# Kernel tuning notes

Measured on AMD Instinct MI355X. Metric: run time of the kernel, lower is better.

Reference implementation:

```python
import jax, jax.numpy as jnp
import numpy as np

NHEAD = 8
LN_EPS = 1e-5   # torch nn.LayerNorm default
ATT_EPS = 1e-6  # LinearAttention eps


def layernorm(x, g, b):
    mu = jnp.mean(x, axis=-1, keepdims=True)
    var = jnp.mean((x - mu) ** 2, axis=-1, keepdims=True)
    return (x - mu) / jnp.sqrt(var + LN_EPS) * g + b


def setup_inputs() -> dict:
    key = jax.random.key(0)
    ks = jax.random.split(key, 9)
    B, C, H, W = 8, 256, 64, 64
    d = C
    w = lambda k, shp: (jax.random.normal(k, shp, dtype=jnp.float32) * 0.02)
    return {
        "x": jax.random.normal(ks[0], (B, C, H, W), dtype=jnp.float32),
        "source": jax.random.normal(ks[1], (B, C, H, W), dtype=jnp.float32),
        # weights stored [in, out] (already transposed vs torch's [out, in])
        "Wq": w(ks[2], (d, d)),
        "Wk": w(ks[3], (d, d)),
        "Wv": w(ks[4], (d, d)),
        "Wm": w(ks[5], (d, d)),
        "W1": w(ks[6], (2 * d, 2 * d)),
        "W2": w(ks[7], (2 * d, d)),
        "g1": jnp.ones((d,), jnp.float32),
        "b1": jnp.zeros((d,), jnp.float32),
        "g2": jnp.ones((d,), jnp.float32),
        "b2": jnp.zeros((d,), jnp.float32),
    }


def reference(x, source, Wq, Wk, Wv, Wm, W1, W2, g1, b1, g2, b2):
    B, C, H, W = x.shape
    L = H * W
    dim = C // NHEAD
    xs = x.reshape(B, C, L).transpose(0, 2, 1)        # [B, L, C]
    ss = source.reshape(B, C, L).transpose(0, 2, 1)   # [B, L, C]

    q = (xs @ Wq).reshape(B, L, NHEAD, dim)
    k = (ss @ Wk).reshape(B, L, NHEAD, dim)
    v = (ss @ Wv).reshape(B, L, NHEAD, dim)

    # linear attention with elu+1 feature map
    Q = jax.nn.elu(q) + 1.0
    K = jax.nn.elu(k) + 1.0
    vals = v / L
    KV = jnp.einsum('nshd,nshv->nhdv', K, vals)                    # [B, h, d, d]
    Z = 1.0 / (jnp.einsum('nlhd,nhd->nlh', Q, K.sum(axis=1)) + ATT_EPS)
    msg = jnp.einsum('nlhd,nhdv,nlh->nlhv', Q, KV, Z) * L          # [B, L, h, d]

    msg = msg.reshape(B, L, C) @ Wm
    msg = layernorm(msg, g1, b1)
    msg = jax.nn.relu(jnp.concatenate([xs, msg], axis=-1) @ W1) @ W2
    msg = layernorm(msg, g2, b2)

    out = xs + msg
    return out.transpose(0, 2, 1).reshape(B, C, H, W)
```

## Files before the change

### kernel.cpp

```cpp
#include <hip/hip_runtime.h>

typedef unsigned short u16;
typedef __bf16 bf16x8 __attribute__((ext_vector_type(8)));
typedef float f32x4 __attribute__((ext_vector_type(4)));

__device__ __forceinline__ u16 f2bf(float f) {
  unsigned int u = __float_as_uint(f);
  u += 0x7fffu + ((u >> 16) & 1u);
  return (u16)(u >> 16);
}
__device__ __forceinline__ float bf2f(u16 v) {
  return __uint_as_float(((unsigned)v) << 16);
}

#define GLDS16(gp, lp)                                                   \
  __builtin_amdgcn_global_load_lds(                                      \
      (const __attribute__((address_space(1))) unsigned int*)(gp),       \
      (__attribute__((address_space(3))) unsigned int*)(lp), 16, 0, 0)

#define OFF_WQ     0u
#define OFF_WK     131072u
#define OFF_WV     262144u
#define OFF_WM     393216u
#define OFF_W1     524288u
#define OFF_W2     1048576u
#define OFF_CAT    1310720u
#define OFF_SSB    34865152u
#define OFF_KVPROJ 68419584u
#define OFF_KV     152305664u
#define OFF_KS     152567808u
#define OFF_KVP    152576000u
#define OFF_KSP    154673152u

__global__ __launch_bounds__(256) void transpose_in_kernel(
    const float* __restrict__ x, const float* __restrict__ srcp,
    u16* __restrict__ cat, u16* __restrict__ ssb) {
  __shared__ float s[32][33];
  int z = blockIdx.z;
  const float* src = z < 8 ? x : srcp;
  u16* dst = z < 8 ? cat : ssb;
  int dstride = z < 8 ? 512 : 256;
  int b = z & 7;
  int lt = blockIdx.x * 32, ct = blockIdx.y * 32;
  int tx = threadIdx.x & 31, ty = threadIdx.x >> 5;
#pragma unroll
  for (int i = 0; i < 4; ++i)
    s[ty + i * 8][tx] = src[((size_t)b * 256 + ct + ty + i * 8) * 4096 + lt + tx];
  __syncthreads();
#pragma unroll
  for (int i = 0; i < 4; ++i)
    dst[((size_t)b * 4096 + lt + ty + i * 8) * dstride + ct + tx] = f2bf(s[tx][ty + i * 8]);
}

__global__ __launch_bounds__(256) void wprep_all_kernel(
    const float* __restrict__ Wq, const float* __restrict__ Wk,
    const float* __restrict__ Wv, const float* __restrict__ Wm,
    const float* __restrict__ W1, const float* __restrict__ W2,
    u16* __restrict__ dq, u16* __restrict__ dk, u16* __restrict__ dv,
    u16* __restrict__ dm, u16* __restrict__ d1, u16* __restrict__ d2) {
  __shared__ float s[32][33];
  int bid = blockIdx.x;
  const float* src; u16* dst; int Kd, Nd, t;
  if (bid < 64)       { src = Wq; dst = dq; Kd = 256; Nd = 256; t = bid; }
  else if (bid < 128) { src = Wk; dst = dk; Kd = 256; Nd = 256; t = bid - 64; }
  else if (bid < 192) { src = Wv; dst = dv; Kd = 256; Nd = 256; t = bid - 128; }
  else if (bid < 256) { src = Wm; dst = dm; Kd = 256; Nd = 256; t = bid - 192; }
  else if (bid < 512) { src = W1; dst = d1; Kd = 512; Nd = 512; t = bid - 256; }
  else                { src = W2; dst = d2; Kd = 512; Nd = 256; t = bid - 512; }
  int ntn = Nd >> 5;
  int kt = (t / ntn) * 32, nt = (t % ntn) * 32;
  int tx = threadIdx.x & 31, ty = threadIdx.x >> 5;
#pragma unroll
  for (int i = 0; i < 4; ++i)
    s[ty + i * 8][tx] = src[(size_t)(kt + ty + i * 8) * Nd + nt + tx];
  __syncthreads();
#pragma unroll
  for (int i = 0; i < 4; ++i)
    dst[(size_t)(nt + ty + i * 8) * Kd + kt + tx] = f2bf(s[tx][ty + i * 8]);
}

template <int EPI>
__global__ __launch_bounds__(512) void gemm256_kernel(
    const u16* __restrict__ A, int lda, const u16* __restrict__ Wt, int K,
    u16* __restrict__ outp, int ldo) {
  __shared__ alignas(16) u16 sA[128 * 64];
  __shared__ alignas(16) u16 sB[256 * 64];
  const int t = threadIdx.x;
  int bid = blockIdx.x;
  int xcd = bid & 7, i0 = bid >> 3;
  const int m0 = (xcd * 32 + (i0 >> 1)) * 128;
  const int n0 = (i0 & 1) * 256;
  const int w = t >> 6, lane = t & 63;
  const int wm = (w >> 2) * 64, wn = (w & 3) * 64;
  const int lr = lane & 15, lk = lane >> 4;
  f32x4 acc[4][4] = {};
  const int nkt = K >> 6;
  for (int kt = 0; kt < nkt; ++kt) {
    __syncthreads();
#pragma unroll
    for (int i = 0; i < 2; ++i) {
      int id = t + i * 512, row = id >> 3, ch = (id & 7) << 3;
      GLDS16(A + (size_t)(m0 + row) * lda + kt * 64 + ch, sA + id * 8);
    }
#pragma unroll
    for (int i = 0; i < 4; ++i) {
      int id = t + i * 512, row = id >> 3, ch = (id & 7) << 3;
      GLDS16(Wt + (size_t)(n0 + row) * K + kt * 64 + ch, sB + id * 8);
    }
    __syncthreads();
    bf16x8 af[4][2], bfr[4][2];
#pragma unroll
    for (int f = 0; f < 4; ++f) {
#pragma unroll
      for (int ks = 0; ks < 2; ++ks) {
        af[f][ks] = *reinterpret_cast<const bf16x8*>(
            &sA[(wm + f * 16 + lr) * 64 + ks * 32 + lk * 8]);
        bfr[f][ks] = *reinterpret_cast<const bf16x8*>(
            &sB[(wn + f * 16 + lr) * 64 + ks * 32 + lk * 8]);
      }
    }
#pragma unroll
    for (int ks = 0; ks < 2; ++ks)
#pragma unroll
      for (int fm = 0; fm < 4; ++fm)
#pragma unroll
        for (int fn = 0; fn < 4; ++fn)
          acc[fm][fn] = __builtin_amdgcn_mfma_f32_16x16x32_bf16(
              af[fm][ks], bfr[fn][ks], acc[fm][fn], 0, 0, 0);
  }
  const int r0 = (lane >> 4) * 4, c0 = lane & 15;
#pragma unroll
  for (int fm = 0; fm < 4; ++fm) {
#pragma unroll
    for (int fn = 0; fn < 4; ++fn) {
      int gr = m0 + wm + fm * 16 + r0;
      int gc = n0 + wn + fn * 16 + c0;
#pragma unroll
      for (int r = 0; r < 4; ++r) {
        float v = acc[fm][fn][r];
        if (EPI == 3) v = v > 0.f ? v : 0.f;
        if (EPI == 4) v = (gc < 256) ? (v > 0.f ? v + 1.f : __expf(v)) : v * (1.f / 4096.f);
        outp[(size_t)(gr + r) * ldo + gc] = f2bf(v);
      }
    }
  }
}

__global__ __launch_bounds__(256) void kv_partial_kernel(
    const u16* __restrict__ KVproj, float* __restrict__ KVp,
    float* __restrict__ KSp) {
  __shared__ alignas(16) float sK[64][32];
  __shared__ alignas(16) float sV[64][32];
  const int bh = blockIdx.x, sl = blockIdx.y;
  const int b = bh >> 3, h = bh & 7;
  const int t = threadIdx.x;
  const int lrow = t >> 2, lcol = (t & 3) * 8;
  const int d = t >> 3, vg = (t & 7) * 4;
  float a0 = 0, a1 = 0, a2 = 0, a3 = 0, ks = 0;
  for (int lt = 0; lt < 512; lt += 64) {
    __syncthreads();
    size_t roff = ((size_t)b * 4096 + sl * 512 + lt + lrow) * 512 + h * 32 + lcol;
    uint4 kq = *reinterpret_cast<const uint4*>(KVproj + roff);
    uint4 vq = *reinterpret_cast<const uint4*>(KVproj + roff + 256);
    float* dk = &sK[lrow][lcol];
    float* dv = &sV[lrow][lcol];
#pragma unroll
    for (int j = 0; j < 4; ++j) {
      unsigned uk = ((const unsigned*)&kq)[j];
      unsigned uv = ((const unsigned*)&vq)[j];
      dk[2 * j] = __uint_as_float(uk << 16);
      dk[2 * j + 1] = __uint_as_float(uk & 0xffff0000u);
      dv[2 * j] = __uint_as_float(uv << 16);
      dv[2 * j + 1] = __uint_as_float(uv & 0xffff0000u);
    }
    __syncthreads();
#pragma unroll 8
    for (int i = 0; i < 64; ++i) {
      float kd = sK[i][d];
      a0 += kd * sV[i][vg + 0];
      a1 += kd * sV[i][vg + 1];
      a2 += kd * sV[i][vg + 2];
      a3 += kd * sV[i][vg + 3];
      ks += kd;
    }
  }
  float* o = KVp + (size_t)sl * 65536 + bh * 1024 + d * 32 + vg;
  o[0] = a0; o[1] = a1; o[2] = a2; o[3] = a3;
  if ((t & 7) == 0) KSp[(size_t)sl * 2048 + bh * 32 + d] = ks;
}

__global__ __launch_bounds__(256) void kv_reduce_kernel(
    const float* __restrict__ KVp, const float* __restrict__ KSp,
    float* __restrict__ KV, float* __restrict__ Ksum) {
  int gid = blockIdx.x * 256 + threadIdx.x;
  if (gid < 65536) {
    float s = 0;
#pragma unroll
    for (int i = 0; i < 8; ++i) s += KVp[(size_t)i * 65536 + gid];
    KV[gid] = s;
  } else if (gid - 65536 < 2048) {
    int j = gid - 65536;
    float s = 0;
#pragma unroll
    for (int i = 0; i < 8; ++i) s += KSp[(size_t)i * 2048 + j];
    Ksum[j] = s;
  }
}

__global__ __launch_bounds__(256) void wcomb_kernel(
    const float* __restrict__ KVb, const u16* __restrict__ wmt,
    u16* __restrict__ wc) {
  const int bid = blockIdx.x;
  const int b = bid >> 8, n = bid & 255;
  const int k = threadIdx.x, h = k >> 5, d = k & 31;
  const float* kv = KVb + ((size_t)b * 8 + h) * 1024 + d * 32;
  const u16* wm = wmt + (size_t)n * 256 + h * 32;
  float s = 0.f;
#pragma unroll
  for (int v = 0; v < 32; ++v) s += kv[v] * bf2f(wm[v]);
  wc[((size_t)b * 256 + n) * 256 + k] = f2bf(s);
}

__global__ __launch_bounds__(256) void qmsg_kernel(
    const u16* __restrict__ cat, const u16* __restrict__ WqT,
    const float* __restrict__ KSb, const u16* __restrict__ wc,
    const float* __restrict__ g1, const float* __restrict__ b1,
    u16* __restrict__ catout) {
  __shared__ alignas(16) char smem[57344];
  u16* sA = (u16*)smem;
  u16* sB = (u16*)(smem + 8192);
  u16* Qlds = (u16*)smem;
  float* scr = (float*)(smem + 33280);
  u16* sWc = (u16*)(smem + 40960);
  u16* T = (u16*)smem;
  const int t = threadIdx.x;
  const int m0 = blockIdx.x * 64;
  const int b = m0 >> 12;
  const int w = t >> 6, lane = t & 63;
  const int lr = lane & 15, lk = lane >> 4;
  const int wn = w * 64;
  f32x4 acc[4][4] = {};
  float ksv[4];
#pragma unroll
  for (int fn = 0; fn < 4; ++fn) ksv[fn] = KSb[b * 256 + wn + fn * 16 + lr];
  for (int kt = 0; kt < 4; ++kt) {
    __syncthreads();
#pragma unroll
    for (int i = 0; i < 2; ++i) {
      int id = t + i * 256, row = id >> 3, ch = (id & 7) * 8;
      GLDS16(cat + (size_t)(m0 + row) * 512 + kt * 64 + ch, sA + id * 8);
    }
#pragma unroll
    for (int i = 0; i < 8; ++i) {
      int id = t + i * 256, row = id >> 3, ch = (id & 7) * 8;
      GLDS16(WqT + (size_t)row * 256 + kt * 64 + ch, sB + id * 8);
    }
    __syncthreads();
    bf16x8 af[4][2], bfr[4][2];
#pragma unroll
    for (int f = 0; f < 4; ++f)
#pragma unroll
      for (int ks = 0; ks < 2; ++ks) {
        af[f][ks] = *(const bf16x8*)&sA[(f * 16 + lr) * 64 + ks * 32 + lk * 8];
        bfr[f][ks] = *(const bf16x8*)&sB[(wn + f * 16 + lr) * 64 + ks * 32 + lk * 8];
      }
#pragma unroll
    for (int ks = 0; ks < 2; ++ks)
#pragma unroll
      for (int fm = 0; fm < 4; ++fm)
#pragma unroll
        for (int fn = 0; fn < 4; ++fn)
          acc[fm][fn] = __builtin_amdgcn_mfma_f32_16x16x32_bf16(
              af[fm][ks], bfr[fn][ks], acc[fm][fn], 0, 0, 0);
  }
#pragma unroll
  for (int fm = 0; fm < 4; ++fm)
#pragma unroll
    for (int r = 0; r < 4; ++r) {
      float q[4];
#pragma unroll
      for (int fn = 0; fn < 4; ++fn) {
        float v = acc[fm][fn][r];
        q[fn] = v > 0.f ? v + 1.f : __expf(v);
      }
      float zd0 = q[0] * ksv[0] + q[1] * ksv[1];
      float zd1 = q[2] * ksv[2] + q[3] * ksv[3];
#pragma unroll
      for (int off = 1; off < 16; off <<= 1) {
        zd0 += __shfl_xor(zd0, off);
        zd1 += __shfl_xor(zd1, off);
      }
      float z0 = 4096.f / (zd0 + 1e-6f);
      float z1 = 4096.f / (zd1 + 1e-6f);
      acc[fm][0][r] = q[0] * z0; acc[fm][1][r] = q[1] * z0;
      acc[fm][2][r] = q[2] * z1; acc[fm][3][r] = q[3] * z1;
    }
  __syncthreads();
#pragma unroll
  for (int fm = 0; fm < 4; ++fm)
#pragma unroll
    for (int fn = 0; fn < 4; ++fn)
#pragma unroll
      for (int r = 0; r < 4; ++r)
        Qlds[(fm * 16 + lk * 4 + r) * 260 + wn + fn * 16 + lr] = f2bf(acc[fm][fn][r]);
  f32x4 acc2[4][4] = {};
  const u16* Bw = wc + (size_t)b * 65536;
  for (int kc = 0; kc < 8; ++kc) {
    __syncthreads();
#pragma unroll
    for (int i = 0; i < 4; ++i) {
      int id = t + i * 256, row = id >> 2, ch = (id & 3) * 8;
      GLDS16(Bw + (size_t)row * 256 + kc * 32 + (ch ^ ((row & 3) << 3)), sWc + id * 8);
    }
    __syncthreads();
    bf16x8 a2[4], b2f[4];
#pragma unroll
    for (int f = 0; f < 4; ++f)
      a2[f] = *(const bf16x8*)&Qlds[(f * 16 + lr) * 260 + kc * 32 + lk * 8];
#pragma unroll
    for (int fn = 0; fn < 4; ++fn) {
      int br = wn + fn * 16 + lr;
      b2f[fn] = *(const bf16x8*)&sWc[br * 32 + ((lk * 8) ^ ((br & 3) << 3))];
    }
#pragma unroll
    for (int fm = 0; fm < 4; ++fm)
#pragma unroll
      for (int fn = 0; fn < 4; ++fn)
        acc2[fm][fn] = __builtin_amdgcn_mfma_f32_16x16x32_bf16(
            a2[fm], b2f[fn], acc2[fm][fn], 0, 0, 0);
  }
#pragma unroll
  for (int fm = 0; fm < 4; ++fm)
#pragma unroll
    for (int r = 0; r < 4; ++r) {
      float s = 0.f, sq = 0.f;
#pragma unroll
      for (int fn = 0; fn < 4; ++fn) {
        float a = acc2[fm][fn][r];
        s += a; sq += a * a;
      }
#pragma unroll
      for (int off = 1; off < 16; off <<= 1) {
        s += __shfl_xor(s, off);
        sq += __shfl_xor(sq, off);
      }
      if (lr == 0) {
        int row = fm * 16 + lk * 4 + r;
        scr[row * 8 + w * 2] = s;
        scr[row * 8 + w * 2 + 1] = sq;
      }
    }
  __syncthreads();
  float gvs[4], bvs[4];
#pragma unroll
  for (int fn = 0; fn < 4; ++fn) {
    gvs[fn] = g1[wn + fn * 16 + lr];
    bvs[fn] = b1[wn + fn * 16 + lr];
  }
#pragma unroll
  for (int fm = 0; fm < 4; ++fm)
#pragma unroll
    for (int r = 0; r < 4; ++r) {
      int row = fm * 16 + lk * 4 + r;
      float s = 0.f, sq = 0.f;
#pragma unroll
      for (int j = 0; j < 4; ++j) {
        s += scr[row * 8 + j * 2];
        sq += scr[row * 8 + j * 2 + 1];
      }
      float mu = s * (1.f / 256.f);
      float var = sq * (1.f / 256.f) - mu * mu;
      float rstd = rsqrtf(var + 1e-5f);
#pragma unroll
      for (int fn = 0; fn < 4; ++fn) {
        float y = (acc2[fm][fn][r] - mu) * rstd * gvs[fn] + bvs[fn];
        T[(fm * 16 + lk * 4 + r) * 260 + wn + fn * 16 + lr] = f2bf(y);
      }
    }
  __syncthreads();
#pragma unroll
  for (int i = 0; i < 8; ++i) {
    int idx = t + i * 256;
    int row = idx >> 5, c16 = idx & 31;
    uint4 val = *reinterpret_cast<const uint4*>(&T[row * 260 + c16 * 8]);
    *reinterpret_cast<uint4*>(catout + (size_t)(m0 + row) * 512 + 256 + c16 * 8) = val;
  }
}

__global__ __launch_bounds__(512) void mlp2_tail_kernel(
    const u16* __restrict__ hidden, const u16* __restrict__ W2T,
    const float* __restrict__ g2, const float* __restrict__ b2,
    const u16* __restrict__ catp, float* __restrict__ out) {
  __shared__ alignas(16) char smem[16384 + 32768 + 4096 + 2048];
  u16* sA = (u16*)smem;
  u16* sB = (u16*)(smem + 16384);
  float* scr = (float*)(smem + 49152);
  float* sG = (float*)(smem + 53248);
  float* T = (float*)smem;
  const int t = threadIdx.x;
  const int m0 = blockIdx.x * 128;
  const int b = m0 >> 12, l0 = m0 & 4095;
  if (t < 256) { sG[t] = g2[t]; sG[256 + t] = b2[t]; }
  const int w = t >> 6, lane = t & 63;
  const int wm = (w >> 2) * 64, wn = (w & 3) * 64;
  const int lr = lane & 15, lk = lane >> 4;
  f32x4 acc[4][4] = {};
  for (int kt = 0; kt < 8; ++kt) {
    __syncthreads();
#pragma unroll
    for (int i = 0; i < 2; ++i) {
      int id = t + i * 512, row = id >> 3, chn = (id & 7) << 3;
      GLDS16(hidden + (size_t)(m0 + row) * 512 + kt * 64 + chn, sA + id * 8);
    }
#pragma unroll
    for (int i = 0; i < 4; ++i) {
      int id = t + i * 512, row = id >> 3, chn = (id & 7) << 3;
      GLDS16(W2T + (size_t)row * 512 + kt * 64 + chn, sB + id * 8);
    }
    __syncthreads();
    bf16x8 af[4][2], bfr[4][2];
#pragma unroll
    for (int f = 0; f < 4; ++f) {
#pragma unroll
      for (int ks = 0; ks < 2; ++ks) {
        af[f][ks] = *reinterpret_cast<const bf16x8*>(
            &sA[(wm + f * 16 + lr) * 64 + ks * 32 + lk * 8]);
        bfr[f][ks] = *reinterpret_cast<const bf16x8*>(
            &sB[(wn + f * 16 + lr) * 64 + ks * 32 + lk * 8]);
      }
    }
#pragma unroll
    for (int ks = 0; ks < 2; ++ks)
#pragma unroll
      for (int fm = 0; fm < 4; ++fm)
#pragma unroll
        for (int fn = 0; fn < 4; ++fn)
          acc[fm][fn] = __builtin_amdgcn_mfma_f32_16x16x32_bf16(
              af[fm][ks], bfr[fn][ks], acc[fm][fn], 0, 0, 0);
  }
#pragma unroll
  for (int fm = 0; fm < 4; ++fm)
#pragma unroll
    for (int r = 0; r < 4; ++r) {
      float s = 0.f, sq = 0.f;
#pragma unroll
      for (int fn = 0; fn < 4; ++fn) {
        float a = acc[fm][fn][r];
        s += a; sq += a * a;
      }
#pragma unroll
      for (int off = 1; off < 16; off <<= 1) {
        s += __shfl_xor(s, off);
        sq += __shfl_xor(sq, off);
      }
      if (lr == 0) {
        int row = wm + fm * 16 + lk * 4 + r;
        scr[row * 8 + (w & 3) * 2] = s;
        scr[row * 8 + (w & 3) * 2 + 1] = sq;
      }
    }
  __syncthreads();
  float gvs[4], bvs[4];
#pragma unroll
  for (int fn = 0; fn < 4; ++fn) {
    gvs[fn] = sG[wn + fn * 16 + lr];
    bvs[fn] = sG[256 + wn + fn * 16 + lr];
  }
#pragma unroll
  for (int fm = 0; fm < 4; ++fm)
#pragma unroll
    for (int r = 0; r < 4; ++r) {
      int row = wm + fm * 16 + lk * 4 + r;
      float s = 0.f, sq = 0.f;
#pragma unroll
      for (int j = 0; j < 4; ++j) {
        s += scr[row * 8 + j * 2];
        sq += scr[row * 8 + j * 2 + 1];
      }
      float mu = s * (1.f / 256.f);
      float var = sq * (1.f / 256.f) - mu * mu;
      float rstd = rsqrtf(var + 1e-5f);
#pragma unroll
      for (int fn = 0; fn < 4; ++fn) {
        float xs = bf2f(catp[(size_t)(m0 + row) * 512 + wn + fn * 16 + lr]);
        acc[fm][fn][r] = (acc[fm][fn][r] - mu) * rstd * gvs[fn] + bvs[fn] + xs;
      }
    }
  __syncthreads();
  for (int cc = 0; cc < 4; ++cc) {
    if ((w & 3) == cc) {
#pragma unroll
      for (int fm = 0; fm < 4; ++fm)
#pragma unroll
        for (int fn = 0; fn < 4; ++fn)
#pragma unroll
          for (int r = 0; r < 4; ++r)
            T[(fn * 16 + lr) * 129 + wm + fm * 16 + lk * 4 + r] = acc[fm][fn][r];
    }
    __syncthreads();
#pragma unroll
    for (int i = 0; i < 4; ++i) {
      int idx = t + i * 512;
      int cT = idx >> 5, lq = (idx & 31) * 4;
      int cg = cc * 64 + cT;
      size_t o = ((size_t)b * 256 + cg) * 4096 + l0 + lq;
      float4 ov;
      ov.x = T[cT * 129 + lq];
      ov.y = T[cT * 129 + lq + 1];
      ov.z = T[cT * 129 + lq + 2];
      ov.w = T[cT * 129 + lq + 3];
      *reinterpret_cast<float4*>(out + o) = ov;
    }
    __syncthreads();
  }
}

extern "C" void kernel_launch(void* const* d_in, const int* in_sizes, int n_in,
                              void* d_out, int out_size, void* d_ws, size_t ws_size,
                              hipStream_t stream) {
  (void)in_sizes; (void)n_in; (void)out_size; (void)ws_size;
  const float* x = (const float*)d_in[0];
  const float* srcp = (const float*)d_in[1];
  const float* Wq = (const float*)d_in[2];
  const float* Wk = (const float*)d_in[3];
  const float* Wv = (const float*)d_in[4];
  const float* Wm = (const float*)d_in[5];
  const float* W1 = (const float*)d_in[6];
  const float* W2 = (const float*)d_in[7];
  const float* g1 = (const float*)d_in[8];
  const float* b1 = (const float*)d_in[9];
  const float* g2 = (const float*)d_in[10];
  const float* b2 = (const float*)d_in[11];
  float* out = (float*)d_out;
  char* ws = (char*)d_ws;

  u16* wqt = (u16*)(ws + OFF_WQ);
  u16* wkvt = (u16*)(ws + OFF_WK);
  u16* wkt = (u16*)(ws + OFF_WK);
  u16* wvt = (u16*)(ws + OFF_WV);
  u16* wmt = (u16*)(ws + OFF_WM);
  u16* w1t = (u16*)(ws + OFF_W1);
  u16* w2t = (u16*)(ws + OFF_W2);
  u16* cat = (u16*)(ws + OFF_CAT);
  u16* ssb = (u16*)(ws + OFF_SSB);
  u16* kvproj = (u16*)(ws + OFF_KVPROJ);
  float* KVb = (float*)(ws + OFF_KV);
  float* KSb = (float*)(ws + OFF_KS);
  float* KVp = (float*)(ws + OFF_KVP);
  float* KSp = (float*)(ws + OFF_KSP);
  u16* hidden = kvproj;
  u16* wcombT = (u16*)(ws + OFF_KVP);

  dim3 blk(256);
  wprep_all_kernel<<<dim3(640), blk, 0, stream>>>(Wq, Wk, Wv, Wm, W1, W2,
                                                  wqt, wkt, wvt, wmt, w1t, w2t);
  transpose_in_kernel<<<dim3(128, 8, 16), blk, 0, stream>>>(x, srcp, cat, ssb);
  gemm256_kernel<4><<<dim3(512), dim3(512), 0, stream>>>(ssb, 256, wkvt, 256, kvproj, 512);
  kv_partial_kernel<<<dim3(64, 8), blk, 0, stream>>>(kvproj, KVp, KSp);
  kv_reduce_kernel<<<dim3(264), blk, 0, stream>>>(KVp, KSp, KVb, KSb);
  wcomb_kernel<<<dim3(2048), blk, 0, stream>>>(KVb, wmt, wcombT);
  qmsg_kernel<<<dim3(512), blk, 0, stream>>>(cat, wqt, KSb, wcombT, g1, b1, cat);
  gemm256_kernel<3><<<dim3(512), dim3(512), 0, stream>>>(cat, 512, w1t, 512, hidden, 512);
  mlp2_tail_kernel<<<dim3(256), dim3(512), 0, stream>>>(hidden, w2t, g2, b2, cat, out);
}
```

Baseline: 161.1 us.

## Fuse KV reduce with Wm combine, widen qmsg tile, vectorize input transpose

The input transpose moves to 64x64 tiles with float4 loads and packed 16-byte bf16 stores. The KV partial reduction and the KV·Wm combine are merged into one kernel that keeps reduced KV in shared memory, which removes a launch and the global KV round trip. The qmsg kernel now processes 128 rows per block with 512 threads, stages Q through LDS in two halves, and writes LayerNorm output directly to global memory instead of through an LDS transpose. In exchange, the fused reduce runs on only 64 blocks, and the direct stores are narrower and less coalesced.

```diff
diff --git a/kernel.cpp b/kernel.cpp
--- a/kernel.cpp
+++ b/kernel.cpp
@@ -27,29 +27,48 @@
 #define OFF_CAT    1310720u
 #define OFF_SSB    34865152u
 #define OFF_KVPROJ 68419584u
-#define OFF_KV     152305664u
 #define OFF_KS     152567808u
 #define OFF_KVP    152576000u
 #define OFF_KSP    154673152u
+#define OFF_WC     154740736u
 
 __global__ __launch_bounds__(256) void transpose_in_kernel(
     const float* __restrict__ x, const float* __restrict__ srcp,
     u16* __restrict__ cat, u16* __restrict__ ssb) {
-  __shared__ float s[32][33];
-  int z = blockIdx.z;
+  __shared__ float s[64][65];
+  const int z = blockIdx.z;
   const float* src = z < 8 ? x : srcp;
   u16* dst = z < 8 ? cat : ssb;
-  int dstride = z < 8 ? 512 : 256;
-  int b = z & 7;
-  int lt = blockIdx.x * 32, ct = blockIdx.y * 32;
-  int tx = threadIdx.x & 31, ty = threadIdx.x >> 5;
-#pragma unroll
-  for (int i = 0; i < 4; ++i)
-    s[ty + i * 8][tx] = src[((size_t)b * 256 + ct + ty + i * 8) * 4096 + lt + tx];
+  const int dstride = z < 8 ? 512 : 256;
+  const int b = z & 7;
+  const int lt = blockIdx.x * 64, ct = blockIdx.y * 64;
+  const int t = threadIdx.x;
+  const int cl = t >> 2, loff = (t & 3) * 16;
+#pragma unroll
+  for (int j = 0; j < 4; ++j) {
+    float4 v = *reinterpret_cast<const float4*>(
+        src + ((size_t)b * 256 + ct + cl) * 4096 + lt + loff + j * 4);
+    s[cl][loff + j * 4 + 0] = v.x;
+    s[cl][loff + j * 4 + 1] = v.y;
+    s[cl][loff + j * 4 + 2] = v.z;
+    s[cl][loff + j * 4 + 3] = v.w;
+  }
   __syncthreads();
 #pragma unroll
-  for (int i = 0; i < 4; ++i)
-    dst[((size_t)b * 4096 + lt + ty + i * 8) * dstride + ct + tx] = f2bf(s[tx][ty + i * 8]);
+  for (int i = 0; i < 2; ++i) {
+    int id = t + i * 256;
+    int ll = id >> 3, cg = id & 7;
+    unsigned pk[4];
+#pragma unroll
+    for (int j = 0; j < 4; ++j) {
+      unsigned lo = f2bf(s[cg * 8 + j * 2][ll]);
+      unsigned hi = f2bf(s[cg * 8 + j * 2 + 1][ll]);
+      pk[j] = lo | (hi << 16);
+    }
+    uint4 val = {pk[0], pk[1], pk[2], pk[3]};
+    *reinterpret_cast<uint4*>(
+        dst + ((size_t)b * 4096 + lt + ll) * dstride + ct + cg * 8) = val;
+  }
 }
 
 __global__ __launch_bounds__(256) void wprep_all_kernel(
@@ -189,56 +208,74 @@
   if ((t & 7) == 0) KSp[(size_t)sl * 2048 + bh * 32 + d] = ks;
 }
 
-__global__ __launch_bounds__(256) void kv_reduce_kernel(
+__global__ __launch_bounds__(256) void kvred_wcomb_kernel(
     const float* __restrict__ KVp, const float* __restrict__ KSp,
-    float* __restrict__ KV, float* __restrict__ Ksum) {
-  int gid = blockIdx.x * 256 + threadIdx.x;
-  if (gid < 65536) {
-    float s = 0;
-#pragma unroll
-    for (int i = 0; i < 8; ++i) s += KVp[(size_t)i * 65536 + gid];
-    KV[gid] = s;
-  } else if (gid - 65536 < 2048) {
-    int j = gid - 65536;
-    float s = 0;
-#pragma unroll
-    for (int i = 0; i < 8; ++i) s += KSp[(size_t)i * 2048 + j];
-    Ksum[j] = s;
-  }
-}
-
-__global__ __launch_bounds__(256) void wcomb_kernel(
-    const float* __restrict__ KVb, const u16* __restrict__ wmt,
-    u16* __restrict__ wc) {
-  const int bid = blockIdx.x;
-  const int b = bid >> 8, n = bid & 255;
-  const int k = threadIdx.x, h = k >> 5, d = k & 31;
-  const float* kv = KVb + ((size_t)b * 8 + h) * 1024 + d * 32;
-  const u16* wm = wmt + (size_t)n * 256 + h * 32;
-  float s = 0.f;
-#pragma unroll
-  for (int v = 0; v < 32; ++v) s += kv[v] * bf2f(wm[v]);
-  wc[((size_t)b * 256 + n) * 256 + k] = f2bf(s);
-}
-
-__global__ __launch_bounds__(256) void qmsg_kernel(
+    const u16* __restrict__ wmt, u16* __restrict__ wc,
+    float* __restrict__ Ksum) {
+  __shared__ float sKV[8 * 1032];
+  const int b = blockIdx.x >> 3, nc = blockIdx.x & 7;
+  const int t = threadIdx.x;
+#pragma unroll
+  for (int i = 0; i < 32; ++i) {
+    int idx = t + i * 256;
+    float s = 0.f;
+#pragma unroll
+    for (int sl = 0; sl < 8; ++sl) s += KVp[(size_t)sl * 65536 + b * 8192 + idx];
+    sKV[(idx >> 10) * 1032 + (idx & 1023)] = s;
+  }
+  if (nc == 0) {
+    float s = 0.f;
+#pragma unroll
+    for (int sl = 0; sl < 8; ++sl) s += KSp[(size_t)sl * 2048 + b * 256 + t];
+    Ksum[b * 256 + t] = s;
+  }
+  __syncthreads();
+  const int n = nc * 32 + (t >> 3), h = t & 7;
+  float wmv[32];
+  const u16* wmrow = wmt + (size_t)n * 256 + h * 32;
+#pragma unroll
+  for (int v = 0; v < 32; ++v) wmv[v] = bf2f(wmrow[v]);
+  unsigned pk[16];
+  const float* kvh = &sKV[h * 1032];
+#pragma unroll
+  for (int dp = 0; dp < 16; ++dp) {
+    unsigned lohi[2];
+#pragma unroll
+    for (int e = 0; e < 2; ++e) {
+      int d = dp * 2 + e;
+      const float* kv = kvh + d * 32;
+      float s = 0.f;
+#pragma unroll
+      for (int v = 0; v < 32; ++v) s += kv[v] * wmv[v];
+      lohi[e] = f2bf(s);
+    }
+    pk[dp] = lohi[0] | (lohi[1] << 16);
+  }
+  uint4* dst = (uint4*)(wc + ((size_t)b * 256 + n) * 256 + h * 32);
+#pragma unroll
+  for (int j = 0; j < 4; ++j) {
+    uint4 val = {pk[j * 4], pk[j * 4 + 1], pk[j * 4 + 2], pk[j * 4 + 3]};
+    dst[j] = val;
+  }
+}
+
+__global__ __launch_bounds__(512) void qmsg_kernel(
     const u16* __restrict__ cat, const u16* __restrict__ WqT,
     const float* __restrict__ KSb, const u16* __restrict__ wc,
     const float* __restrict__ g1, const float* __restrict__ b1,
     u16* __restrict__ catout) {
   __shared__ alignas(16) char smem[57344];
   u16* sA = (u16*)smem;
-  u16* sB = (u16*)(smem + 8192);
+  u16* sB = (u16*)(smem + 16384);
   u16* Qlds = (u16*)smem;
-  float* scr = (float*)(smem + 33280);
-  u16* sWc = (u16*)(smem + 40960);
-  u16* T = (u16*)smem;
+  u16* sWc = (u16*)(smem + 35840);
+  float* scr = (float*)(smem + 52224);
   const int t = threadIdx.x;
-  const int m0 = blockIdx.x * 64;
+  const int m0 = blockIdx.x * 128;
   const int b = m0 >> 12;
   const int w = t >> 6, lane = t & 63;
+  const int wm = (w >> 2) * 64, wn = (w & 3) * 64;
   const int lr = lane & 15, lk = lane >> 4;
-  const int wn = w * 64;
   f32x4 acc[4][4] = {};
   float ksv[4];
 #pragma unroll
@@ -247,12 +284,12 @@
     __syncthreads();
 #pragma unroll
     for (int i = 0; i < 2; ++i) {
-      int id = t + i * 256, row = id >> 3, ch = (id & 7) * 8;
+      int id = t + i * 512, row = id >> 3, ch = (id & 7) << 3;
       GLDS16(cat + (size_t)(m0 + row) * 512 + kt * 64 + ch, sA + id * 8);
     }
 #pragma unroll
-    for (int i = 0; i < 8; ++i) {
-      int id = t + i * 256, row = id >> 3, ch = (id & 7) * 8;
+    for (int i = 0; i < 4; ++i) {
+      int id = t + i * 512, row = id >> 3, ch = (id & 7) << 3;
       GLDS16(WqT + (size_t)row * 256 + kt * 64 + ch, sB + id * 8);
     }
     __syncthreads();
@@ -261,7 +298,7 @@
     for (int f = 0; f < 4; ++f)
 #pragma unroll
       for (int ks = 0; ks < 2; ++ks) {
-        af[f][ks] = *(const bf16x8*)&sA[(f * 16 + lr) * 64 + ks * 32 + lk * 8];
+        af[f][ks] = *(const bf16x8*)&sA[(wm + f * 16 + lr) * 64 + ks * 32 + lk * 8];
         bfr[f][ks] = *(const bf16x8*)&sB[(wn + f * 16 + lr) * 64 + ks * 32 + lk * 8];
       }
 #pragma unroll
@@ -295,39 +332,46 @@
       acc[fm][0][r] = q[0] * z0; acc[fm][1][r] = q[1] * z0;
       acc[fm][2][r] = q[2] * z1; acc[fm][3][r] = q[3] * z1;
     }
-  __syncthreads();
-#pragma unroll
-  for (int fm = 0; fm < 4; ++fm)
-#pragma unroll
-    for (int fn = 0; fn < 4; ++fn)
-#pragma unroll
-      for (int r = 0; r < 4; ++r)
-        Qlds[(fm * 16 + lk * 4 + r) * 260 + wn + fn * 16 + lr] = f2bf(acc[fm][fn][r]);
   f32x4 acc2[4][4] = {};
   const u16* Bw = wc + (size_t)b * 65536;
-  for (int kc = 0; kc < 8; ++kc) {
-    __syncthreads();
-#pragma unroll
-    for (int i = 0; i < 4; ++i) {
-      int id = t + i * 256, row = id >> 2, ch = (id & 3) * 8;
-      GLDS16(Bw + (size_t)row * 256 + kc * 32 + (ch ^ ((row & 3) << 3)), sWc + id * 8);
-    }
-    __syncthreads();
-    bf16x8 a2[4], b2f[4];
-#pragma unroll
-    for (int f = 0; f < 4; ++f)
-      a2[f] = *(const bf16x8*)&Qlds[(f * 16 + lr) * 260 + kc * 32 + lk * 8];
-#pragma unroll
-    for (int fn = 0; fn < 4; ++fn) {
-      int br = wn + fn * 16 + lr;
-      b2f[fn] = *(const bf16x8*)&sWc[br * 32 + ((lk * 8) ^ ((br & 3) << 3))];
-    }
-#pragma unroll
-    for (int fm = 0; fm < 4; ++fm)
-#pragma unroll
-      for (int fn = 0; fn < 4; ++fn)
-        acc2[fm][fn] = __builtin_amdgcn_mfma_f32_16x16x32_bf16(
-            a2[fm], b2f[fn], acc2[fm][fn], 0, 0, 0);
+  for (int hh = 0; hh < 2; ++hh) {
+    __syncthreads();
+    if ((wn >> 7) == hh) {
+#pragma unroll
+      for (int fm = 0; fm < 4; ++fm)
+#pragma unroll
+        for (int fn = 0; fn < 4; ++fn)
+#pragma unroll
+          for (int r = 0; r < 4; ++r)
+            Qlds[(wm + fm * 16 + lk * 4 + r) * 136 + (wn & 64) + fn * 16 + lr] =
+                f2bf(acc[fm][fn][r]);
+    }
+    __syncthreads();
+    for (int kc2 = 0; kc2 < 4; ++kc2) {
+#pragma unroll
+      for (int i = 0; i < 2; ++i) {
+        int id = t + i * 512, row = id >> 2, ch = (id & 3) << 3;
+        GLDS16(Bw + (size_t)row * 256 + hh * 128 + kc2 * 32 +
+                   (ch ^ ((row & 3) << 3)), sWc + id * 8);
+      }
+      __syncthreads();
+      bf16x8 a2[4], b2f[4];
+#pragma unroll
+      for (int f = 0; f < 4; ++f)
+        a2[f] = *(const bf16x8*)&Qlds[(wm + f * 16 + lr) * 136 + kc2 * 32 + lk * 8];
+#pragma unroll
+      for (int fn = 0; fn < 4; ++fn) {
+        int br = wn + fn * 16 + lr;
+        b2f[fn] = *(const bf16x8*)&sWc[br * 32 + ((lk * 8) ^ ((br & 3) << 3))];
+      }
+#pragma unroll
+      for (int fm = 0; fm < 4; ++fm)
+#pragma unroll
+        for (int fn = 0; fn < 4; ++fn)
+          acc2[fm][fn] = __builtin_amdgcn_mfma_f32_16x16x32_bf16(
+              a2[fm], b2f[fn], acc2[fm][fn], 0, 0, 0);
+      __syncthreads();
+    }
   }
 #pragma unroll
   for (int fm = 0; fm < 4; ++fm)
@@ -345,9 +389,9 @@
         sq += __shfl_xor(sq, off);
       }
       if (lr == 0) {
-        int row = fm * 16 + lk * 4 + r;
-        scr[row * 8 + w * 2] = s;
-        scr[row * 8 + w * 2 + 1] = sq;
+        int row = wm + fm * 16 + lk * 4 + r;
+        scr[row * 8 + (w & 3) * 2] = s;
+        scr[row * 8 + (w & 3) * 2 + 1] = sq;
       }
     }
   __syncthreads();
@@ -361,7 +405,7 @@
   for (int fm = 0; fm < 4; ++fm)
 #pragma unroll
     for (int r = 0; r < 4; ++r) {
-      int row = fm * 16 + lk * 4 + r;
+      int row = wm + fm * 16 + lk * 4 + r;
       float s = 0.f, sq = 0.f;
 #pragma unroll
       for (int j = 0; j < 4; ++j) {
@@ -374,17 +418,9 @@
 #pragma unroll
       for (int fn = 0; fn < 4; ++fn) {
         float y = (acc2[fm][fn][r] - mu) * rstd * gvs[fn] + bvs[fn];
-        T[(fm * 16 + lk * 4 + r) * 260 + wn + fn * 16 + lr] = f2bf(y);
-      }
-    }
-  __syncthreads();
-#pragma unroll
-  for (int i = 0; i < 8; ++i) {
-    int idx = t + i * 256;
-    int row = idx >> 5, c16 = idx & 31;
-    uint4 val = *reinterpret_cast<const uint4*>(&T[row * 260 + c16 * 8]);
-    *reinterpret_cast<uint4*>(catout + (size_t)(m0 + row) * 512 + 256 + c16 * 8) = val;
-  }
+        catout[(size_t)(m0 + row) * 512 + 256 + wn + fn * 16 + lr] = f2bf(y);
+      }
+    }
 }
 
 __global__ __launch_bounds__(512) void mlp2_tail_kernel(
@@ -544,22 +580,20 @@
   u16* cat = (u16*)(ws + OFF_CAT);
   u16* ssb = (u16*)(ws + OFF_SSB);
   u16* kvproj = (u16*)(ws + OFF_KVPROJ);
-  float* KVb = (float*)(ws + OFF_KV);
   float* KSb = (float*)(ws + OFF_KS);
   float* KVp = (float*)(ws + OFF_KVP);
   float* KSp = (float*)(ws + OFF_KSP);
+  u16* wcombT = (u16*)(ws + OFF_WC);
   u16* hidden = kvproj;
-  u16* wcombT = (u16*)(ws + OFF_KVP);
 
   dim3 blk(256);
   wprep_all_kernel<<<dim3(640), blk, 0, stream>>>(Wq, Wk, Wv, Wm, W1, W2,
                                                   wqt, wkt, wvt, wmt, w1t, w2t);
-  transpose_in_kernel<<<dim3(128, 8, 16), blk, 0, stream>>>(x, srcp, cat, ssb);
+  transpose_in_kernel<<<dim3(64, 4, 16), blk, 0, stream>>>(x, srcp, cat, ssb);
   gemm256_kernel<4><<<dim3(512), dim3(512), 0, stream>>>(ssb, 256, wkvt, 256, kvproj, 512);
   kv_partial_kernel<<<dim3(64, 8), blk, 0, stream>>>(kvproj, KVp, KSp);
-  kv_reduce_kernel<<<dim3(264), blk, 0, stream>>>(KVp, KSp, KVb, KSb);
-  wcomb_kernel<<<dim3(2048), blk, 0, stream>>>(KVb, wmt, wcombT);
-  qmsg_kernel<<<dim3(512), blk, 0, stream>>>(cat, wqt, KSb, wcombT, g1, b1, cat);
+  kvred_wcomb_kernel<<<dim3(64), blk, 0, stream>>>(KVp, KSp, wmt, wcombT, KSb);
+  qmsg_kernel<<<dim3(256), dim3(512), 0, stream>>>(cat, wqt, KSb, wcombT, g1, b1, cat);
   gemm256_kernel<3><<<dim3(512), dim3(512), 0, stream>>>(cat, 512, w1t, 512, hidden, 512);
   mlp2_tail_kernel<<<dim3(256), dim3(512), 0, stream>>>(hidden, w2t, g2, b2, cat, out);
 }
```

Measured after the change: 158.6 us. No clear change (-1.6%).
